# Kernel optimization log

Measured on AMD Instinct MI355X. Metric: run time of the kernel, lower is better.

## Reference

```python
import jax, jax.numpy as jnp
import numpy as np

B, N, D = 4, 2048, 256
EPS = 1e-5


def _clinear(Z, W, b):
    # complex linear: Z (B,2,N,din), W (2,dout,din), b (2,dout)
    Zr, Zi = Z[:, 0], Z[:, 1]
    Wr, Wi = W[0], W[1]
    outr = Zr @ Wr.T - Zi @ Wi.T + b[0]
    outi = Zr @ Wi.T + Zi @ Wr.T + b[1]
    return jnp.stack([outr, outi], axis=1)


def setup_inputs() -> dict:
    key = jax.random.key(0)
    ks = jax.random.split(key, 14)
    sc = 1.0 / np.sqrt(D).astype(np.float32)
    t = jnp.tile(jnp.arange(N + 1, dtype=jnp.float32)[None] * 0.01, (B, 1))
    return {
        'Z_q': jax.random.normal(ks[0], (B, 2, N, D), jnp.float32),
        'Z_k': jax.random.normal(ks[1], (B, 2, N, D), jnp.float32),
        'Z_v': jax.random.normal(ks[2], (B, 2, N, D), jnp.float32),
        't_measure_all': t,
        'W_q': jax.random.normal(ks[3], (2, D, D), jnp.float32) * sc,
        'b_q': jax.random.normal(ks[4], (2, D), jnp.float32) * 0.01,
        'W_k': jax.random.normal(ks[5], (2, D, D), jnp.float32) * sc,
        'b_k': jax.random.normal(ks[6], (2, D), jnp.float32) * 0.01,
        'W_v': jax.random.normal(ks[7], (2, D, D), jnp.float32) * sc,
        'b_v': jax.random.normal(ks[8], (2, D), jnp.float32) * 0.01,
        'W_p': jax.random.normal(ks[9], (2, D, D), jnp.float32) * sc,
        'b_p': jax.random.normal(ks[10], (2, D), jnp.float32) * 0.01,
        'lambda1': jax.random.normal(ks[11], (2, D // 2, 1), jnp.float32),
        'lambda_Omega_sqrt': jax.random.normal(ks[12], (1, D, 1), jnp.float32) * sc,
        'lambda_Gamma_sqrt': jax.random.normal(ks[13], (1, D, 1), jnp.float32) * sc,
        'tau': jnp.asarray(1.0, jnp.float32),
        'delta': jnp.asarray(0.0, jnp.float32),
        'lambda_C': jnp.ones((1, D, 1), jnp.float32),
    }


def reference(Z_q, Z_k, Z_v, t_measure_all, W_q, b_q, W_k, b_k, W_v, b_v,
              W_p, b_p, lambda1, lambda_Omega_sqrt, lambda_Gamma_sqrt,
              tau, delta, lambda_C):
    # lambda_h = 0 * compute_lambda_h(lambda1): conjugate-pair spectrum, zeroed in forward
    lam_r = 0.0 * jnp.concatenate([lambda1[0], lambda1[0]], axis=0)[:, 0]   # (D,)
    lam_i = 0.0 * jnp.concatenate([lambda1[1], -lambda1[1]], axis=0)[:, 0]  # (D,)
    lam_Om = lambda_Omega_sqrt ** 2 + EPS   # process noise (1,D,1)
    lam_Ga = lambda_Gamma_sqrt ** 2 + EPS   # measurement noise (1,D,1)

    Q = _clinear(Z_q, W_q, b_q)  # (B,2,N,D)
    K = _clinear(Z_k, W_k, b_k)
    V = _clinear(Z_v, W_v, b_v)

    t = t_measure_all[0, :-1]  # (N,)
    # exponential state-transition kernels exp(+/- lambda * t): (2,N,D)
    mag_f = jnp.exp(lam_r[None] * t[:, None]); ph_f = lam_i[None] * t[:, None]
    exp_f = jnp.stack([mag_f * jnp.cos(ph_f), mag_f * jnp.sin(ph_f)])
    mag_b = jnp.exp(-lam_r[None] * t[:, None]); ph_b = -lam_i[None] * t[:, None]
    exp_b = jnp.stack([mag_b * jnp.cos(ph_b), mag_b * jnp.sin(ph_b)])
    # one-step transition exp(lambda * dt): (2,D)
    dt = t[1] - t[0]
    mat_exp = jnp.stack([jnp.exp(lam_r * dt) * jnp.cos(lam_i * dt),
                         jnp.exp(lam_r * dt) * jnp.sin(lam_i * dt)])

    # averaged covariance kernel, exact lambda->0 limit: Gamma + Omega*|t_i-t_j|, mean over D
    lamC2 = lambda_C[0, :, 0] ** 2
    ga_bar = jnp.mean(lamC2 * lam_Ga[0, :, 0])
    om_bar = jnp.mean(lamC2 * lam_Om[0, :, 0])
    abs_dt = jnp.abs(t[:, None] - t[None, :])          # (N,N)
    V_avg_ij = ga_bar + om_bar * abs_dt                # (N,N)

    # factorized kernels
    V_v = exp_f[None]                 # (1,2,N,D)
    U_q = exp_b[None] * Q             # (B,2,N,D)
    U_k = exp_b[None] * K
    U_v = exp_b[None] * V

    # precision-weighted squared residual norm R_ij = sum_d |V_k|^2 |U_q_i - U_k_j|^2
    Vk_abs = jnp.sum(exp_f ** 2, axis=0)              # (N,D)
    Uk_abs = jnp.sum(U_k ** 2, axis=1)                # (B,N,D)
    Uq_abs = jnp.sum(U_q ** 2, axis=1)                # (B,N,D)
    T1 = jnp.einsum('id,bjd->bij', Vk_abs, Uk_abs)
    T2 = jnp.sum(Vk_abs[None] * Uq_abs, axis=2)[:, :, None]
    T3 = (jnp.einsum('bid,bjd->bij', Vk_abs[None] * U_q[:, 0], U_k[:, 0]) +
          jnp.einsum('bid,bjd->bij', Vk_abs[None] * U_q[:, 1], U_k[:, 1]))
    R_qk_abs = T1 + T2 - 2.0 * T3                     # (B,N,N)

    scores = -(tau ** 2) * jnp.log(V_avg_ij[None] + R_qk_abs)
    mask = jnp.tril(jnp.ones((N, N), bool))
    scores = jnp.where(mask[None], scores, -jnp.inf)
    A = jax.nn.softmax(scores, axis=2)                # (B,N,N)
    Q_ij = jnp.stack([A, jnp.zeros_like(A)], axis=1)  # (B,2,N,N)

    # est_inner = complex matmul(Q_ij, U_v); Q imag part is zero
    est_inner = jnp.stack([jnp.einsum('bij,bjd->bid', A, U_v[:, 0]),
                           jnp.einsum('bij,bjd->bid', A, U_v[:, 1])], axis=1)
    est_v = V_v * est_inner          # plain elementwise product, as in source
    s = jax.nn.sigmoid(delta)
    est_eigenbasis = (1.0 - s) * V + s * est_v        # (B,2,N,D)

    # complex Hadamard with one-step transition
    pr = mat_exp[0][None, None] * est_eigenbasis[:, 0] - mat_exp[1][None, None] * est_eigenbasis[:, 1]
    pi = mat_exp[0][None, None] * est_eigenbasis[:, 1] + mat_exp[1][None, None] * est_eigenbasis[:, 0]
    pred_p = jnp.stack([pr, pi], axis=1)
    out = _clinear(pred_p, W_p, b_p)                  # (B,2,N,D)

    lambda_h = jnp.stack([lam_r, lam_i])[..., None]
    return est_eigenbasis, out, Q_ij, V_v, U_v, lambda_h
```

## Files before the change

kernel.cpp:

```cpp
#include <hip/hip_runtime.h>
#include <math.h>

#define BN 4
#define NN 2048
#define DD 256
#define EPSF 1e-5f

typedef __attribute__((ext_vector_type(8))) short bf16x8;
typedef __attribute__((ext_vector_type(4))) float f32x4;

constexpr size_t OFF_EST = 0;
constexpr size_t OFF_OUT = (size_t)BN * 2 * NN * DD;
constexpr size_t OFF_QIJ = OFF_OUT + (size_t)BN * 2 * NN * DD;
constexpr size_t OFF_VV  = OFF_QIJ + (size_t)BN * 2 * NN * NN;
constexpr size_t OFF_UV  = OFF_VV + (size_t)2 * NN * DD;
constexpr size_t OFF_LH  = OFF_UV + (size_t)BN * 2 * NN * DD;

constexpr size_t SCR_B0   = OFF_QIJ + (size_t)NN * NN;
constexpr size_t U_Q16    = 0;
constexpr size_t U_K16    = (size_t)BN * NN * DD;
constexpr size_t U_VT16   = 2 * (size_t)BN * NN * DD;
constexpr size_t SCR_QN   = SCR_B0 + 3 * (size_t)BN * NN * DD / 2;
constexpr size_t SCR_KN   = SCR_QN + (size_t)BN * NN;
constexpr size_t SCR_L    = SCR_KN + (size_t)BN * NN;
constexpr size_t SCR_SC   = SCR_L + (size_t)BN * NN;
constexpr size_t SCR_W16P = SCR_SC + 16;
constexpr size_t SCR_E16F = OFF_QIJ + 3 * (size_t)NN * NN;
constexpr size_t U_PART   = (size_t)BN * NN * 512;
constexpr size_t SCR_Z16F = OFF_QIJ + 5 * (size_t)NN * NN;
constexpr size_t SCR_Z16VF = OFF_QIJ + 7 * (size_t)NN * NN;
constexpr size_t U_W16    = (size_t)BN * NN * 512;

__device__ __forceinline__ short f2bf(float x) {
    union { float f; unsigned u; } v; v.f = x;
    unsigned r = v.u + 0x7fff + ((v.u >> 16) & 1);
    return (short)(r >> 16);
}
__device__ __forceinline__ float bf2f(unsigned short h) {
    union { unsigned u; float f; } v; v.u = ((unsigned)h) << 16;
    return v.f;
}
__device__ __forceinline__ unsigned short* u16p(float* d, size_t fofs) {
    return (unsigned short*)(d + fofs);
}
__device__ __forceinline__ const unsigned short* u16pc(const float* d, size_t fofs) {
    return (const unsigned short*)(d + fofs);
}
__device__ __forceinline__ int nc_of(int TI) { return TI >= 12 ? 3 : (TI >= 6 ? 2 : 1); }
__device__ __forceinline__ int cb_of(int TI) {
    return TI < 6 ? TI : (TI < 12 ? 6 + 2 * (TI - 6) : 18 + 3 * (TI - 12));
}

__global__ void k_cvt(const float* __restrict__ Zq, const float* __restrict__ Zk,
                      const float* __restrict__ Zv,
                      const float* __restrict__ Wq, const float* __restrict__ Wk,
                      const float* __restrict__ Wv, const float* __restrict__ Wp,
                      const float* __restrict__ tau, const float* __restrict__ delta,
                      const float* __restrict__ lamOm, const float* __restrict__ lamGa,
                      const float* __restrict__ lamC,
                      float* __restrict__ dout) {
    const int z = blockIdx.z;
    if (z < 3) {
        const float* Z = (z == 0) ? Zq : (z == 1) ? Zk : Zv;
        unsigned short* O = (z == 0) ? u16p(dout, SCR_Z16F)
                          : (z == 1) ? u16p(dout, SCR_Z16F) + (size_t)BN * NN * 512
                                     : u16p(dout, SCR_Z16VF);
        const long n4 = (long)BN * 2 * NN * DD / 4;
        for (long i4 = (long)blockIdx.x * 256 + threadIdx.x; i4 < n4;
             i4 += (long)gridDim.x * 256) {
            const long i = i4 * 4;
            const int d = (int)(i & (DD - 1));
            const long r = i >> 8;
            const int n = (int)(r & (NN - 1));
            const long bc = r >> 11;
            const int c = (int)(bc & 1), b = (int)(bc >> 1);
            float4 v = *(const float4*)&Z[i];
            ushort4 o;
            o.x = (unsigned short)f2bf(v.x); o.y = (unsigned short)f2bf(v.y);
            o.z = (unsigned short)f2bf(v.z); o.w = (unsigned short)f2bf(v.w);
            *(ushort4*)&O[((size_t)(b * NN + n)) * 512 + c * 256 + d] = o;
        }
    } else if (z == 3) {
        const float* Ws[4] = {Wq, Wk, Wv, Wp};
        const long n4 = 6L * 256 * 512 / 4;
        for (long e4 = (long)blockIdx.x * 256 + threadIdx.x; e4 < n4;
             e4 += (long)gridDim.x * 256) {
            const long e = e4 * 4;
            const int k = (int)(e & 511);
            const long rest = e >> 9;
            const int dd = (int)(rest & 255);
            const int m = (int)(rest >> 8);
            int proj, mode;
            if (m < 3)      { proj = m; mode = 0; }
            else if (m == 3){ proj = 2; mode = 1; }
            else            { proj = 3; mode = m - 4; }
            const int kc = k >> 8, kk = k & 255;
            int wc; float sgn;
            if (mode == 0) { wc = kc; sgn = kc ? -1.f : 1.f; }
            else           { wc = 1 - kc; sgn = 1.f; }
            float4 v = *(const float4*)&Ws[proj][((size_t)wc * DD + dd) * DD + kk];
            ushort4 o;
            o.x = (unsigned short)f2bf(sgn * v.x); o.y = (unsigned short)f2bf(sgn * v.y);
            o.z = (unsigned short)f2bf(sgn * v.z); o.w = (unsigned short)f2bf(sgn * v.w);
            unsigned short* dst = (m < 4)
                ? u16p(dout, SCR_Z16VF) + U_W16 + (size_t)m * 131072
                : u16p(dout, SCR_W16P) + (size_t)(m - 4) * 131072;
            *(ushort4*)&dst[(size_t)dd * 512 + k] = o;
        }
    } else {
        const int idx = blockIdx.x * 256 + threadIdx.x;
        if (idx < 3 * BN * NN) dout[SCR_QN + idx] = 0.f;
        if (blockIdx.x == 0) {
            __shared__ float red[8];
            const int t = threadIdx.x;
            float c2 = lamC[t] * lamC[t];
            float ga = c2 * (lamGa[t] * lamGa[t] + EPSF);
            float om = c2 * (lamOm[t] * lamOm[t] + EPSF);
            for (int o = 32; o > 0; o >>= 1) {
                ga += __shfl_down(ga, o, 64);
                om += __shfl_down(om, o, 64);
            }
            if ((t & 63) == 0) { red[t >> 6] = ga; red[4 + (t >> 6)] = om; }
            __syncthreads();
            if (t == 0) {
                float gs = red[0] + red[1] + red[2] + red[3];
                float os = red[4] + red[5] + red[6] + red[7];
                float* scal = dout + SCR_SC;
                scal[0] = tau[0] * tau[0];
                scal[1] = 1.f / (1.f + __expf(-delta[0]));
                scal[2] = gs / 256.f;
                scal[3] = os / 256.f;
            }
        }
    }
}

__global__ __launch_bounds__(256) void k_qkv(const float* __restrict__ bq,
                                             const float* __restrict__ bk,
                                             const float* __restrict__ bv,
                                             float* __restrict__ dout)
{
    __shared__ short Al[128 * 40];
    __shared__ short Bl[128 * 40];
    const int z = blockIdx.z;
    const int d0 = blockIdx.x * 128;
    const int b = blockIdx.y >> 4;
    const int n0 = (blockIdx.y & 15) * 128;

    const unsigned short* Z16 =
        (z == 0) ? u16pc(dout, SCR_Z16F)
      : (z == 1) ? u16pc(dout, SCR_Z16F) + (size_t)BN * NN * 512
                 : u16pc(dout, SCR_Z16VF);
    const unsigned short* W16 = u16pc(dout, SCR_Z16VF) + U_W16 + (size_t)z * 131072;
    const float* bias = (z == 0) ? bq : (z == 1) ? bk : bv;
    const int bofs = (z == 3) ? DD : 0;

    const int t = threadIdx.x, wave = t >> 6, lane = t & 63, quad = lane >> 4, lm = lane & 15;
    const int wm = (wave >> 1) * 64, wn = (wave & 1) * 64;
    const int srow = t >> 1, sch = (t & 1) * 16;

    f32x4 acc[4][4];
#pragma unroll
    for (int i = 0; i < 4; ++i)
#pragma unroll
        for (int j = 0; j < 4; ++j) acc[i][j] = (f32x4){0.f, 0.f, 0.f, 0.f};

    for (int kt = 0; kt < 16; ++kt) {
        const int kk0 = kt * 32;
        const unsigned short* Za = Z16 + ((size_t)(b * NN + n0 + srow)) * 512 + kk0 + sch;
        bf16x8 a0 = *(const bf16x8*)(Za + 0);
        bf16x8 a1 = *(const bf16x8*)(Za + 8);
        const unsigned short* Wa = W16 + (size_t)(d0 + srow) * 512 + kk0 + sch;
        bf16x8 w0 = *(const bf16x8*)(Wa + 0);
        bf16x8 w1 = *(const bf16x8*)(Wa + 8);
        __syncthreads();
        *(bf16x8*)&Al[srow * 40 + sch]     = a0;
        *(bf16x8*)&Al[srow * 40 + sch + 8] = a1;
        *(bf16x8*)&Bl[srow * 40 + sch]     = w0;
        *(bf16x8*)&Bl[srow * 40 + sch + 8] = w1;
        __syncthreads();
        bf16x8 af[4], bff[4];
#pragma unroll
        for (int mi = 0; mi < 4; ++mi) af[mi] = *(const bf16x8*)&Al[(wm + mi * 16 + lm) * 40 + quad * 8];
#pragma unroll
        for (int nj = 0; nj < 4; ++nj) bff[nj] = *(const bf16x8*)&Bl[(wn + nj * 16 + lm) * 40 + quad * 8];
#pragma unroll
        for (int mi = 0; mi < 4; ++mi)
#pragma unroll
            for (int nj = 0; nj < 4; ++nj)
                acc[mi][nj] = __builtin_amdgcn_mfma_f32_16x16x32_bf16(af[mi], bff[nj], acc[mi][nj], 0, 0, 0);
    }

    if (z <= 1) {
        unsigned short* O16 = u16p(dout, SCR_B0) + (z ? U_K16 : U_Q16) + (size_t)b * NN * DD;
        float* NRM = dout + (z ? SCR_KN : SCR_QN) + b * NN;
#pragma unroll
        for (int mi = 0; mi < 4; ++mi)
#pragma unroll
            for (int r = 0; r < 4; ++r) {
                const int m = n0 + wm + mi * 16 + quad * 4 + r;
                float ss = 0.f;
#pragma unroll
                for (int nj = 0; nj < 4; ++nj) {
                    const int d = d0 + wn + nj * 16 + lm;
                    unsigned short h = (unsigned short)f2bf(acc[mi][nj][r] + bias[d]);
                    O16[(size_t)m * DD + d] = h;
                    const float vb = bf2f(h);
                    ss = fmaf(vb, vb, ss);
                }
                ss += __shfl_down(ss, 8, 16); ss += __shfl_down(ss, 4, 16);
                ss += __shfl_down(ss, 2, 16); ss += __shfl_down(ss, 1, 16);
                if (lm == 0) atomicAdd(&NRM[m], ss);
            }
    } else if (z == 2) {
        float* UV0 = dout + OFF_UV + (size_t)(b * 2) * NN * DD;
#pragma unroll
        for (int mi = 0; mi < 4; ++mi)
#pragma unroll
            for (int r = 0; r < 4; ++r) {
                const int m = n0 + wm + mi * 16 + quad * 4 + r;
#pragma unroll
                for (int nj = 0; nj < 4; ++nj) {
                    const int d = d0 + wn + nj * 16 + lm;
                    UV0[(size_t)m * DD + d] = acc[mi][nj][r] + bias[d];
                }
            }
    } else {
        const float s1 = 1.f - dout[SCR_SC + 1];
        float* EST1 = dout + OFF_EST + (size_t)(b * 2 + 1) * NN * DD;
        unsigned short* E16 = u16p(dout, SCR_E16F) + (size_t)b * NN * 512;
#pragma unroll
        for (int mi = 0; mi < 4; ++mi)
#pragma unroll
            for (int r = 0; r < 4; ++r) {
                const int m = n0 + wm + mi * 16 + quad * 4 + r;
#pragma unroll
                for (int nj = 0; nj < 4; ++nj) {
                    const int d = d0 + wn + nj * 16 + lm;
                    const float v = s1 * (acc[mi][nj][r] + bias[bofs + d]);
                    EST1[(size_t)m * DD + d] = v;
                    E16[(size_t)m * 512 + 256 + d] = (unsigned short)f2bf(v);
                }
            }
    }
}

__global__ __launch_bounds__(256) void k_outproj(const float* __restrict__ bp,
                                                 float* __restrict__ dout)
{
    __shared__ short Al[128 * 40];
    __shared__ short Bl[128 * 40];
    const int z = blockIdx.z;
    const int d0 = blockIdx.x * 128;
    const int b = blockIdx.y >> 4;
    const int n0 = (blockIdx.y & 15) * 128;
    const unsigned short* E16 = u16pc(dout, SCR_E16F) + (size_t)b * NN * 512;
    const unsigned short* W16 = u16pc(dout, SCR_W16P) + (size_t)z * 131072;

    const int t = threadIdx.x, wave = t >> 6, lane = t & 63, quad = lane >> 4, lm = lane & 15;
    const int wm = (wave >> 1) * 64, wn = (wave & 1) * 64;
    const int srow = t >> 1, sch = (t & 1) * 16;

    f32x4 acc[4][4];
#pragma unroll
    for (int i = 0; i < 4; ++i)
#pragma unroll
        for (int j = 0; j < 4; ++j) acc[i][j] = (f32x4){0.f, 0.f, 0.f, 0.f};

    for (int kt = 0; kt < 16; ++kt) {
        const int kk0 = kt * 32;
        const unsigned short* Za = E16 + ((size_t)(n0 + srow)) * 512 + kk0 + sch;
        bf16x8 a0 = *(const bf16x8*)(Za + 0);
        bf16x8 a1 = *(const bf16x8*)(Za + 8);
        const unsigned short* Wa = W16 + (size_t)(d0 + srow) * 512 + kk0 + sch;
        bf16x8 w0 = *(const bf16x8*)(Wa + 0);
        bf16x8 w1 = *(const bf16x8*)(Wa + 8);
        __syncthreads();
        *(bf16x8*)&Al[srow * 40 + sch]     = a0;
        *(bf16x8*)&Al[srow * 40 + sch + 8] = a1;
        *(bf16x8*)&Bl[srow * 40 + sch]     = w0;
        *(bf16x8*)&Bl[srow * 40 + sch + 8] = w1;
        __syncthreads();
        bf16x8 af[4], bff[4];
#pragma unroll
        for (int mi = 0; mi < 4; ++mi) af[mi] = *(const bf16x8*)&Al[(wm + mi * 16 + lm) * 40 + quad * 8];
#pragma unroll
        for (int nj = 0; nj < 4; ++nj) bff[nj] = *(const bf16x8*)&Bl[(wn + nj * 16 + lm) * 40 + quad * 8];
#pragma unroll
        for (int mi = 0; mi < 4; ++mi)
#pragma unroll
            for (int nj = 0; nj < 4; ++nj)
                acc[mi][nj] = __builtin_amdgcn_mfma_f32_16x16x32_bf16(af[mi], bff[nj], acc[mi][nj], 0, 0, 0);
    }
    const int bofs = z ? DD : 0;
    float* O = dout + OFF_OUT + (size_t)(b * 2 + z) * NN * DD;
#pragma unroll
    for (int mi = 0; mi < 4; ++mi)
#pragma unroll
        for (int r = 0; r < 4; ++r) {
            const int m = n0 + wm + mi * 16 + quad * 4 + r;
#pragma unroll
            for (int nj = 0; nj < 4; ++nj) {
                const int d = d0 + wn + nj * 16 + lm;
                O[(size_t)m * DD + d] = acc[mi][nj][r] + bp[bofs + d];
            }
        }
}

__global__ void k_vtrans(float* __restrict__ dout) {
    __shared__ float T[64][65];
    const int b = blockIdx.z;
    const int nb = blockIdx.x * 64, db = blockIdx.y * 64;
    const float* V = dout + OFF_UV + (size_t)(b * 2) * NN * DD;
    unsigned short* VT = u16p(dout, SCR_B0) + U_VT16 + (size_t)b * DD * NN;
    const int tr = threadIdx.x >> 4, tc = (threadIdx.x & 15) * 4;
#pragma unroll
    for (int p = 0; p < 4; ++p) {
        float4 v = *(const float4*)&V[(size_t)(nb + tr + p * 16) * DD + db + tc];
        T[tr + p * 16][tc + 0] = v.x; T[tr + p * 16][tc + 1] = v.y;
        T[tr + p * 16][tc + 2] = v.z; T[tr + p * 16][tc + 3] = v.w;
    }
    __syncthreads();
#pragma unroll
    for (int p = 0; p < 4; ++p) {
        const int d = tr + p * 16;
        ushort4 o;
        o.x = (unsigned short)f2bf(T[tc + 0][d]);
        o.y = (unsigned short)f2bf(T[tc + 1][d]);
        o.z = (unsigned short)f2bf(T[tc + 2][d]);
        o.w = (unsigned short)f2bf(T[tc + 3][d]);
        *(ushort4*)&VT[(size_t)(db + d) * NN + nb + tc] = o;
    }
}

__global__ __launch_bounds__(256) void k_scores(const float* __restrict__ tmeas,
                                                float* __restrict__ dout) {
    __shared__ short Al[128 * 40];
    __shared__ short Bl[128 * 40];
    const int b = blockIdx.y, x = blockIdx.x;
    int ti = (int)((sqrtf(8.f * x + 1.f) - 1.f) * 0.5f);
    while ((ti + 1) * (ti + 2) / 2 <= x) ++ti;
    while (ti * (ti + 1) / 2 > x) --ti;
    const int tj = x - ti * (ti + 1) / 2;
    const int i0 = ti * 128, j0 = tj * 128;
    const unsigned short* Q16 = u16pc(dout, SCR_B0) + U_Q16 + (size_t)b * NN * DD;
    const unsigned short* K16 = u16pc(dout, SCR_B0) + U_K16 + (size_t)b * NN * DD;
    const int t = threadIdx.x, wave = t >> 6, lane = t & 63, quad = lane >> 4, lm = lane & 15;
    const int wm = (wave >> 1) * 64, wn = (wave & 1) * 64;
    const int srow = t >> 1, sch = (t & 1) * 16;

    f32x4 acc[4][4];
#pragma unroll
    for (int i = 0; i < 4; ++i)
#pragma unroll
        for (int j = 0; j < 4; ++j) acc[i][j] = (f32x4){0.f, 0.f, 0.f, 0.f};

    for (int kt = 0; kt < 8; ++kt) {
        const int kk0 = kt * 32;
        bf16x8 q0 = *(const bf16x8*)(Q16 + (size_t)(i0 + srow) * DD + kk0 + sch);
        bf16x8 q1 = *(const bf16x8*)(Q16 + (size_t)(i0 + srow) * DD + kk0 + sch + 8);
        bf16x8 k0 = *(const bf16x8*)(K16 + (size_t)(j0 + srow) * DD + kk0 + sch);
        bf16x8 k1 = *(const bf16x8*)(K16 + (size_t)(j0 + srow) * DD + kk0 + sch + 8);
        __syncthreads();
        *(bf16x8*)&Al[srow * 40 + sch]     = q0;
        *(bf16x8*)&Al[srow * 40 + sch + 8] = q1;
        *(bf16x8*)&Bl[srow * 40 + sch]     = k0;
        *(bf16x8*)&Bl[srow * 40 + sch + 8] = k1;
        __syncthreads();
        bf16x8 af[4], bff[4];
#pragma unroll
        for (int mi = 0; mi < 4; ++mi) af[mi] = *(const bf16x8*)&Al[(wm + mi * 16 + lm) * 40 + quad * 8];
#pragma unroll
        for (int nj = 0; nj < 4; ++nj) bff[nj] = *(const bf16x8*)&Bl[(wn + nj * 16 + lm) * 40 + quad * 8];
#pragma unroll
        for (int mi = 0; mi < 4; ++mi)
#pragma unroll
            for (int nj = 0; nj < 4; ++nj)
                acc[mi][nj] = __builtin_amdgcn_mfma_f32_16x16x32_bf16(af[mi], bff[nj], acc[mi][nj], 0, 0, 0);
    }

    const float tau2 = dout[SCR_SC + 0], ga = dout[SCR_SC + 2], om = dout[SCR_SC + 3];
    float* Qij = dout + OFF_QIJ + (size_t)b * 2 * NN * NN;
    const float* QN_ = dout + SCR_QN + b * NN;
    const float* KN_ = dout + SCR_KN + b * NN;
    float kn[4], tjv[4]; int jj[4];
#pragma unroll
    for (int nj = 0; nj < 4; ++nj) {
        jj[nj] = j0 + wn + nj * 16 + lm;
        kn[nj] = KN_[jj[nj]];
        tjv[nj] = tmeas[jj[nj]];
    }
#pragma unroll
    for (int mi = 0; mi < 4; ++mi)
#pragma unroll
        for (int r = 0; r < 4; ++r) {
            const int i = i0 + wm + mi * 16 + quad * 4 + r;
            const float qni = QN_[i], tqi = tmeas[i];
            float rs = 0.f;
#pragma unroll
            for (int nj = 0; nj < 4; ++nj) {
                float xx = ga + om * fabsf(tqi - tjv[nj]) + qni + kn[nj] - 2.f * acc[mi][nj][r];
                xx = fmaxf(xx, 1e-30f);
                float w = (tau2 == 1.f) ? (1.f / xx) : __expf(-tau2 * __logf(xx));
                if (jj[nj] > i) w = 0.f;
                Qij[(size_t)i * NN + jj[nj]] = w;
                rs += w;
            }
            rs += __shfl_down(rs, 8, 16); rs += __shfl_down(rs, 4, 16);
            rs += __shfl_down(rs, 2, 16); rs += __shfl_down(rs, 1, 16);
            if (lm == 0) atomicAdd(&dout[SCR_L + b * NN + i], rs);
        }
}

__global__ __launch_bounds__(512) void k_estinner(float* __restrict__ dout) {
    __shared__ short Al[128 * 40];
    __shared__ short Bl[256 * 40];
    const int b = blockIdx.y;
    int y = blockIdx.x, TI = 0, cb = 0;
    for (;;) { const int nc = nc_of(TI); if (y < nc) break; y -= nc; cb += nc; ++TI; }
    const int i0 = TI * 128;
    const int kbeg = y * 768;
    const int kend = min(kbeg + 768, (TI + 1) * 128);
    const int nst = (kend - kbeg) >> 5;
    const int cidx = cb + y;
    float* Qij = dout + OFF_QIJ + (size_t)b * 2 * NN * NN;
    const unsigned short* VT = u16pc(dout, SCR_B0) + U_VT16 + (size_t)b * DD * NN;

    const int t = threadIdx.x, wave = t >> 6, lane = t & 63, quad = lane >> 4, lm = lane & 15;
    const int wm = (wave >> 2) * 64, wn = (wave & 3) * 64;
    const int arow = t >> 2, acol = (t & 3) * 8;
    const int vrow = t >> 1, vcol = (t & 1) * 16;
    const float linv = 1.f / dout[SCR_L + b * NN + i0 + arow];

    f32x4 acc[4][4];
#pragma unroll
    for (int i = 0; i < 4; ++i)
#pragma unroll
        for (int j = 0; j < 4; ++j) acc[i][j] = (f32x4){0.f, 0.f, 0.f, 0.f};

    for (int kt = 0; kt < nst; ++kt) {
        const int kk0 = kbeg + kt * 32;
        float* Ap = &Qij[(size_t)(i0 + arow) * NN + kk0 + acol];
        float4 w0 = *(const float4*)(Ap + 0);
        float4 w1 = *(const float4*)(Ap + 4);
        w0.x *= linv; w0.y *= linv; w0.z *= linv; w0.w *= linv;
        w1.x *= linv; w1.y *= linv; w1.z *= linv; w1.w *= linv;
        bf16x8 pa;
        pa[0] = f2bf(w0.x); pa[1] = f2bf(w0.y); pa[2] = f2bf(w0.z); pa[3] = f2bf(w0.w);
        pa[4] = f2bf(w1.x); pa[5] = f2bf(w1.y); pa[6] = f2bf(w1.z); pa[7] = f2bf(w1.w);
        bf16x8 v0 = *(const bf16x8*)(VT + (size_t)vrow * NN + kk0 + vcol);
        bf16x8 v1 = *(const bf16x8*)(VT + (size_t)vrow * NN + kk0 + vcol + 8);
        *(float4*)(Ap + 0) = w0;
        *(float4*)(Ap + 4) = w1;
        __syncthreads();
        *(bf16x8*)&Al[arow * 40 + acol] = pa;
        *(bf16x8*)&Bl[vrow * 40 + vcol]     = v0;
        *(bf16x8*)&Bl[vrow * 40 + vcol + 8] = v1;
        __syncthreads();
        bf16x8 af[4], bff[4];
#pragma unroll
        for (int mi = 0; mi < 4; ++mi) af[mi] = *(const bf16x8*)&Al[(wm + mi * 16 + lm) * 40 + quad * 8];
#pragma unroll
        for (int nj = 0; nj < 4; ++nj) bff[nj] = *(const bf16x8*)&Bl[(wn + nj * 16 + lm) * 40 + quad * 8];
#pragma unroll
        for (int mi = 0; mi < 4; ++mi)
#pragma unroll
            for (int nj = 0; nj < 4; ++nj)
                acc[mi][nj] = __builtin_amdgcn_mfma_f32_16x16x32_bf16(af[mi], bff[nj], acc[mi][nj], 0, 0, 0);
    }
    unsigned short* P = u16p(dout, SCR_E16F) + U_PART +
                        ((size_t)(b * 30 + cidx)) * 128 * 256;
#pragma unroll
    for (int mi = 0; mi < 4; ++mi)
#pragma unroll
        for (int r = 0; r < 4; ++r) {
            const int ri = wm + mi * 16 + quad * 4 + r;
#pragma unroll
            for (int nj = 0; nj < 4; ++nj) {
                const int d = wn + nj * 16 + lm;
                P[(size_t)ri * 256 + d] = (unsigned short)f2bf(acc[mi][nj][r]);
            }
        }
}

__global__ void k_blendfills(float* __restrict__ dout) {
    const int z = blockIdx.z;
    if (z < 4) {
        const int b = z;
        if (blockIdx.x >= 512) return;
        const int t = threadIdx.x;
        const int i = blockIdx.x * 4 + (t >> 6);
        const int d4 = (t & 63) * 4;
        const int TI = i >> 7;
        const int nc = nc_of(TI), cb = cb_of(TI);
        const float s = dout[SCR_SC + 1];
        const unsigned short* P = u16pc(dout, SCR_E16F) + U_PART;
        float4 sum = {0.f, 0.f, 0.f, 0.f};
        for (int c = 0; c < nc; ++c) {
            ushort4 pv = *(const ushort4*)&P[((size_t)(b * 30 + cb + c) * 128 + (i & 127)) * 256 + d4];
            sum.x += bf2f(pv.x); sum.y += bf2f(pv.y);
            sum.z += bf2f(pv.z); sum.w += bf2f(pv.w);
        }
        const float4 vr = *(const float4*)&dout[OFF_UV + ((size_t)(b * 2) * NN + i) * DD + d4];
        float4 ev;
        ev.x = (1.f - s) * vr.x + s * sum.x;
        ev.y = (1.f - s) * vr.y + s * sum.y;
        ev.z = (1.f - s) * vr.z + s * sum.z;
        ev.w = (1.f - s) * vr.w + s * sum.w;
        *(float4*)&dout[OFF_EST + ((size_t)(b * 2) * NN + i) * DD + d4] = ev;
        ushort4 o;
        o.x = (unsigned short)f2bf(ev.x); o.y = (unsigned short)f2bf(ev.y);
        o.z = (unsigned short)f2bf(ev.z); o.w = (unsigned short)f2bf(ev.w);
        *(ushort4*)&u16p(dout, SCR_E16F)[((size_t)(b * NN + i)) * 512 + d4] = o;
        return;
    }
    if (z < 8) {
        const int b = z - 4, i = blockIdx.x;
        const int jstart = ((i >> 7) + 1) << 7;
        float* row = dout + OFF_QIJ + (size_t)b * 2 * NN * NN + (size_t)i * NN;
        const float4 zz = {0.f, 0.f, 0.f, 0.f};
        for (int j = jstart + threadIdx.x * 4; j < NN; j += 256 * 4)
            *(float4*)&row[j] = zz;
        return;
    }
    size_t base; long n; float val = 0.f;
    if (z == 8)       { base = SCR_B0; n = 3145728; }
    else if (z == 9)  { base = SCR_Z16F; n = (long)NN * NN; }
    else if (z == 10) { base = SCR_Z16VF; n = (long)NN * NN; }
    else if (z == 11) { base = OFF_VV; n = (long)NN * DD; val = 1.f; }
    else if (z == 12) { base = OFF_VV + (size_t)NN * DD; n = (long)NN * DD; }
    else if (z < 17)  { base = OFF_UV + (size_t)(2 * (z - 13) + 1) * NN * DD; n = (long)NN * DD; }
    else              { base = OFF_LH; n = 512; }
    float* p = dout + base;
    const float4 v = {val, val, val, val};
    for (long i = ((long)blockIdx.x * 256 + threadIdx.x) * 4; i < n;
         i += (long)gridDim.x * 1024)
        *(float4*)&p[i] = v;
}

__global__ void k_tail(float* __restrict__ dout) {
    const float4 zz = {0.f, 0.f, 0.f, 0.f};
    const long n1 = (long)NN * NN;
    for (long i = ((long)blockIdx.x * 256 + threadIdx.x) * 4; i < n1;
         i += (long)gridDim.x * 1024)
        *(float4*)&dout[SCR_E16F + i] = zz;
    const long n0 = (long)NN * NN - 3145728;
    for (long i = ((long)blockIdx.x * 256 + threadIdx.x) * 4; i < n0;
         i += (long)gridDim.x * 1024)
        *(float4*)&dout[SCR_QN + i] = zz;
}

extern "C" void kernel_launch(void* const* d_in, const int* in_sizes, int n_in,
                              void* d_out, int out_size, void* d_ws, size_t ws_size,
                              hipStream_t stream) {
    const float* Zq = (const float*)d_in[0];
    const float* Zk = (const float*)d_in[1];
    const float* Zv = (const float*)d_in[2];
    const float* tm = (const float*)d_in[3];
    const float* Wq = (const float*)d_in[4];
    const float* bq = (const float*)d_in[5];
    const float* Wk = (const float*)d_in[6];
    const float* bk = (const float*)d_in[7];
    const float* Wv = (const float*)d_in[8];
    const float* bv = (const float*)d_in[9];
    const float* Wp = (const float*)d_in[10];
    const float* bp = (const float*)d_in[11];
    const float* lamOm = (const float*)d_in[13];
    const float* lamGa = (const float*)d_in[14];
    const float* tau = (const float*)d_in[15];
    const float* delta = (const float*)d_in[16];
    const float* lamC = (const float*)d_in[17];
    float* out = (float*)d_out;

    k_cvt<<<dim3(2048, 1, 5), dim3(256), 0, stream>>>(
        Zq, Zk, Zv, Wq, Wk, Wv, Wp, tau, delta, lamOm, lamGa, lamC, out);
    k_qkv<<<dim3(2, 64, 4), dim3(256), 0, stream>>>(bq, bk, bv, out);
    k_vtrans<<<dim3(32, 4, 4), dim3(256), 0, stream>>>(out);
    k_scores<<<dim3(136, 4), dim3(256), 0, stream>>>(tm, out);
    k_estinner<<<dim3(30, 4), dim3(512), 0, stream>>>(out);
    k_blendfills<<<dim3(2048, 1, 18), dim3(256), 0, stream>>>(out);
    k_outproj<<<dim3(2, 64, 2), dim3(256), 0, stream>>>(bp, out);
    k_tail<<<dim3(2048), dim3(256), 0, stream>>>(out);
}
```

Measured before the change: 353.7 us.

## Stage unnormalized scores as packed bf16 tiles and split est_inner across D halves

k_scores now writes unnormalized attention weights as bf16 into packed 128x128 triangle tiles in scratch instead of fp32 into the full Q_ij output. k_estinner reads these compact tiles and splits the D dimension across two 256-thread blocks, doubling the grid. Only the first half writes the normalized fp32 Q_ij, and the 1/rowsum normalization of the A@V partials moves into the blend kernel. This cuts fp32 read/write traffic on the big N×N matrix and raises parallelism, but Q_ij values now pass through bf16 rounding, and the scratch region reuse must not overlap other buffers.

```diff
diff --git a/kernel.cpp b/kernel.cpp
--- a/kernel.cpp
+++ b/kernel.cpp
@@ -31,6 +31,8 @@
 constexpr size_t SCR_Z16VF = OFF_QIJ + 7 * (size_t)NN * NN;
 constexpr size_t U_W16    = (size_t)BN * NN * 512;
 
+constexpr size_t W16_PER_B = 136 * 16384;
+
 __device__ __forceinline__ short f2bf(float x) {
     union { float f; unsigned u; } v; v.f = x;
     unsigned r = v.u + 0x7fff + ((v.u >> 16) & 1);
@@ -45,6 +47,14 @@
 }
 __device__ __forceinline__ const unsigned short* u16pc(const float* d, size_t fofs) {
     return (const unsigned short*)(d + fofs);
+}
+__device__ __forceinline__ unsigned short* w16p(float* d, int b) {
+    return (b < 3) ? u16p(d, SCR_Z16F) + (size_t)b * W16_PER_B
+                   : u16p(d, SCR_Z16VF);
+}
+__device__ __forceinline__ const unsigned short* w16pc(const float* d, int b) {
+    return (b < 3) ? u16pc(d, SCR_Z16F) + (size_t)b * W16_PER_B
+                   : u16pc(d, SCR_Z16VF);
 }
 __device__ __forceinline__ int nc_of(int TI) { return TI >= 12 ? 3 : (TI >= 6 ? 2 : 1); }
 __device__ __forceinline__ int cb_of(int TI) {
@@ -380,7 +390,7 @@
     }
 
     const float tau2 = dout[SCR_SC + 0], ga = dout[SCR_SC + 2], om = dout[SCR_SC + 3];
-    float* Qij = dout + OFF_QIJ + (size_t)b * 2 * NN * NN;
+    unsigned short* WT = w16p(dout, b) + (size_t)x * 16384;
     const float* QN_ = dout + SCR_QN + b * NN;
     const float* KN_ = dout + SCR_KN + b * NN;
     float kn[4], tjv[4]; int jj[4];
@@ -394,17 +404,20 @@
     for (int mi = 0; mi < 4; ++mi)
 #pragma unroll
         for (int r = 0; r < 4; ++r) {
-            const int i = i0 + wm + mi * 16 + quad * 4 + r;
+            const int li = wm + mi * 16 + quad * 4 + r;
+            const int i = i0 + li;
             const float qni = QN_[i], tqi = tmeas[i];
             float rs = 0.f;
 #pragma unroll
             for (int nj = 0; nj < 4; ++nj) {
                 float xx = ga + om * fabsf(tqi - tjv[nj]) + qni + kn[nj] - 2.f * acc[mi][nj][r];
                 xx = fmaxf(xx, 1e-30f);
-                float w = (tau2 == 1.f) ? (1.f / xx) : __expf(-tau2 * __logf(xx));
+                float w = (tau2 == 1.f) ? __builtin_amdgcn_rcpf(xx)
+                                        : __expf(-tau2 * __logf(xx));
                 if (jj[nj] > i) w = 0.f;
-                Qij[(size_t)i * NN + jj[nj]] = w;
-                rs += w;
+                const unsigned short h = (unsigned short)f2bf(w);
+                WT[(size_t)li * 128 + (wn + nj * 16 + lm)] = h;
+                rs += bf2f(h);
             }
             rs += __shfl_down(rs, 8, 16); rs += __shfl_down(rs, 4, 16);
             rs += __shfl_down(rs, 2, 16); rs += __shfl_down(rs, 1, 16);
@@ -412,25 +425,27 @@
         }
 }
 
-__global__ __launch_bounds__(512) void k_estinner(float* __restrict__ dout) {
+__global__ __launch_bounds__(256) void k_estinner(float* __restrict__ dout) {
     __shared__ short Al[128 * 40];
-    __shared__ short Bl[256 * 40];
+    __shared__ short Bl[128 * 40];
     const int b = blockIdx.y;
-    int y = blockIdx.x, TI = 0, cb = 0;
+    const int chunk = blockIdx.x >> 1, half = blockIdx.x & 1;
+    int y = chunk, TI = 0, cb = 0;
     for (;;) { const int nc = nc_of(TI); if (y < nc) break; y -= nc; cb += nc; ++TI; }
     const int i0 = TI * 128;
     const int kbeg = y * 768;
     const int kend = min(kbeg + 768, (TI + 1) * 128);
     const int nst = (kend - kbeg) >> 5;
     const int cidx = cb + y;
+    const int tri = TI * (TI + 1) / 2;
+    const unsigned short* WT = w16pc(dout, b);
+    const unsigned short* VT = u16pc(dout, SCR_B0) + U_VT16 + (size_t)b * DD * NN;
     float* Qij = dout + OFF_QIJ + (size_t)b * 2 * NN * NN;
-    const unsigned short* VT = u16pc(dout, SCR_B0) + U_VT16 + (size_t)b * DD * NN;
 
     const int t = threadIdx.x, wave = t >> 6, lane = t & 63, quad = lane >> 4, lm = lane & 15;
-    const int wm = (wave >> 2) * 64, wn = (wave & 3) * 64;
-    const int arow = t >> 2, acol = (t & 3) * 8;
-    const int vrow = t >> 1, vcol = (t & 1) * 16;
-    const float linv = 1.f / dout[SCR_L + b * NN + i0 + arow];
+    const int wm = (wave >> 1) * 64, wn = (wave & 1) * 64;
+    const int arow = t >> 1, asel = (t & 1) * 16;
+    const float linv = (half == 0) ? 1.f / dout[SCR_L + b * NN + i0 + arow] : 0.f;
 
     f32x4 acc[4][4];
 #pragma unroll
@@ -440,23 +455,44 @@
 
     for (int kt = 0; kt < nst; ++kt) {
         const int kk0 = kbeg + kt * 32;
-        float* Ap = &Qij[(size_t)(i0 + arow) * NN + kk0 + acol];
-        float4 w0 = *(const float4*)(Ap + 0);
-        float4 w1 = *(const float4*)(Ap + 4);
-        w0.x *= linv; w0.y *= linv; w0.z *= linv; w0.w *= linv;
-        w1.x *= linv; w1.y *= linv; w1.z *= linv; w1.w *= linv;
-        bf16x8 pa;
-        pa[0] = f2bf(w0.x); pa[1] = f2bf(w0.y); pa[2] = f2bf(w0.z); pa[3] = f2bf(w0.w);
-        pa[4] = f2bf(w1.x); pa[5] = f2bf(w1.y); pa[6] = f2bf(w1.z); pa[7] = f2bf(w1.w);
-        bf16x8 v0 = *(const bf16x8*)(VT + (size_t)vrow * NN + kk0 + vcol);
-        bf16x8 v1 = *(const bf16x8*)(VT + (size_t)vrow * NN + kk0 + vcol + 8);
-        *(float4*)(Ap + 0) = w0;
-        *(float4*)(Ap + 4) = w1;
-        __syncthreads();
-        *(bf16x8*)&Al[arow * 40 + acol] = pa;
-        *(bf16x8*)&Bl[vrow * 40 + vcol]     = v0;
-        *(bf16x8*)&Bl[vrow * 40 + vcol + 8] = v1;
-        __syncthreads();
+        const int tile = kk0 >> 7;
+        const unsigned short* Ap = WT + ((size_t)(tri + tile)) * 16384
+                                 + (size_t)arow * 128 + (kk0 & 127) + asel;
+        bf16x8 a0 = *(const bf16x8*)(Ap + 0);
+        bf16x8 a1 = *(const bf16x8*)(Ap + 8);
+        const unsigned short* Vp = VT + (size_t)(half * 128 + arow) * NN + kk0 + asel;
+        bf16x8 v0 = *(const bf16x8*)(Vp + 0);
+        bf16x8 v1 = *(const bf16x8*)(Vp + 8);
+        __syncthreads();
+        *(bf16x8*)&Al[arow * 40 + asel]     = a0;
+        *(bf16x8*)&Al[arow * 40 + asel + 8] = a1;
+        *(bf16x8*)&Bl[arow * 40 + asel]     = v0;
+        *(bf16x8*)&Bl[arow * 40 + asel + 8] = v1;
+        __syncthreads();
+        if (half == 0) {
+            float* Qp = &Qij[(size_t)(i0 + arow) * NN + kk0 + asel];
+            float4 f;
+            f.x = bf2f((unsigned short)a0[0]) * linv;
+            f.y = bf2f((unsigned short)a0[1]) * linv;
+            f.z = bf2f((unsigned short)a0[2]) * linv;
+            f.w = bf2f((unsigned short)a0[3]) * linv;
+            *(float4*)(Qp + 0) = f;
+            f.x = bf2f((unsigned short)a0[4]) * linv;
+            f.y = bf2f((unsigned short)a0[5]) * linv;
+            f.z = bf2f((unsigned short)a0[6]) * linv;
+            f.w = bf2f((unsigned short)a0[7]) * linv;
+            *(float4*)(Qp + 4) = f;
+            f.x = bf2f((unsigned short)a1[0]) * linv;
+            f.y = bf2f((unsigned short)a1[1]) * linv;
+            f.z = bf2f((unsigned short)a1[2]) * linv;
+            f.w = bf2f((unsigned short)a1[3]) * linv;
+            *(float4*)(Qp + 8) = f;
+            f.x = bf2f((unsigned short)a1[4]) * linv;
+            f.y = bf2f((unsigned short)a1[5]) * linv;
+            f.z = bf2f((unsigned short)a1[6]) * linv;
+            f.w = bf2f((unsigned short)a1[7]) * linv;
+            *(float4*)(Qp + 12) = f;
+        }
         bf16x8 af[4], bff[4];
 #pragma unroll
         for (int mi = 0; mi < 4; ++mi) af[mi] = *(const bf16x8*)&Al[(wm + mi * 16 + lm) * 40 + quad * 8];
@@ -477,7 +513,7 @@
             const int ri = wm + mi * 16 + quad * 4 + r;
 #pragma unroll
             for (int nj = 0; nj < 4; ++nj) {
-                const int d = wn + nj * 16 + lm;
+                const int d = half * 128 + wn + nj * 16 + lm;
                 P[(size_t)ri * 256 + d] = (unsigned short)f2bf(acc[mi][nj][r]);
             }
         }
@@ -494,6 +530,7 @@
         const int TI = i >> 7;
         const int nc = nc_of(TI), cb = cb_of(TI);
         const float s = dout[SCR_SC + 1];
+        const float linv = 1.f / dout[SCR_L + b * NN + i];
         const unsigned short* P = u16pc(dout, SCR_E16F) + U_PART;
         float4 sum = {0.f, 0.f, 0.f, 0.f};
         for (int c = 0; c < nc; ++c) {
@@ -502,11 +539,12 @@
             sum.z += bf2f(pv.z); sum.w += bf2f(pv.w);
         }
         const float4 vr = *(const float4*)&dout[OFF_UV + ((size_t)(b * 2) * NN + i) * DD + d4];
+        const float sl = s * linv;
         float4 ev;
-        ev.x = (1.f - s) * vr.x + s * sum.x;
-        ev.y = (1.f - s) * vr.y + s * sum.y;
-        ev.z = (1.f - s) * vr.z + s * sum.z;
-        ev.w = (1.f - s) * vr.w + s * sum.w;
+        ev.x = (1.f - s) * vr.x + sl * sum.x;
+        ev.y = (1.f - s) * vr.y + sl * sum.y;
+        ev.z = (1.f - s) * vr.z + sl * sum.z;
+        ev.w = (1.f - s) * vr.w + sl * sum.w;
         *(float4*)&dout[OFF_EST + ((size_t)(b * 2) * NN + i) * DD + d4] = ev;
         ushort4 o;
         o.x = (unsigned short)f2bf(ev.x); o.y = (unsigned short)f2bf(ev.y);
@@ -577,7 +615,7 @@
     k_qkv<<<dim3(2, 64, 4), dim3(256), 0, stream>>>(bq, bk, bv, out);
     k_vtrans<<<dim3(32, 4, 4), dim3(256), 0, stream>>>(out);
     k_scores<<<dim3(136, 4), dim3(256), 0, stream>>>(tm, out);
-    k_estinner<<<dim3(30, 4), dim3(512), 0, stream>>>(out);
+    k_estinner<<<dim3(60, 4), dim3(256), 0, stream>>>(out);
     k_blendfills<<<dim3(2048, 1, 18), dim3(256), 0, stream>>>(out);
     k_outproj<<<dim3(2, 64, 2), dim3(256), 0, stream>>>(bp, out);
     k_tail<<<dim3(2048), dim3(256), 0, stream>>>(out);
```

After: 354.8 us. Within noise of the previous version (+0.3%).
